# Performance work log

Measured on AMD Instinct MI355X. Metric: run time of the kernel, lower is better.

Reference implementation:

```python
import jax, jax.numpy as jnp
import numpy as np
import math

K, N, T, HID = 10, 96, 40, 48   # samples, agents (batch_size=1), timesteps, hidden
HZ = 10.0
R0, R1 = 0.5, 4.0
SPB = 6                          # social pooling grid is 6x6
RSTEP = (R1 - R0) / SPB          # radius_step (not set in shown source; natural value)
TWO_PI = 2.0 * math.pi
TSTEP = TWO_PI / SPB             # theta_step


def setup_inputs() -> dict:
    key = jax.random.key(0)
    ks = iter(jax.random.split(key, 24))
    def u(shape, fan):
        s = 1.0 / float(np.sqrt(fan))
        return jax.random.uniform(next(ks), shape, jnp.float32, -s, s)
    inp = {
        "hx": jax.random.normal(next(ks), (N, HID), jnp.float32),
        # locations in [-15,15] keep feature-map pixel gather in-bounds (u=40-long(y))
        "current_location": (jax.random.uniform(next(ks), (N, 2), jnp.float32) - 0.5) * 30.0,
        "y_path": (jax.random.uniform(next(ks), (K, T, N, 2), jnp.float32) - 0.5) * 30.0,
        "image_data": jax.random.normal(next(ks), (1, 4, 160, 160), jnp.float32),
        "conv1_w": u((16, 4, 5, 5), 4 * 25), "conv1_b": u((16,), 4 * 25),
        "conv2_w": u((32, 16, 5, 5), 16 * 25), "conv2_b": u((32,), 16 * 25),
        "fcvel_w": u((16, 2), 2), "fcvel_b": u((16,), 2),
        "gru_wih": u((3 * HID, 96), 96), "gru_whh": u((3 * HID, HID), HID),
        "gru_bih": u((3 * HID,), HID), "gru_bhh": u((3 * HID,), HID),
        "fcscf_w": u((HID, SPB * SPB * HID), SPB * SPB * HID), "fcscf_b": u((HID,), SPB * SPB * HID),
        "fcscore_w": u((1, HID), HID), "fcscore_b": u((1,), HID),
        "fcdy_w": u((2 * T, HID), HID), "fcdy_b": u((2 * T,), HID),
    }
    return inp


def _forward(hx, current_location, y_path, image_data, conv1_w, conv1_b, conv2_w, conv2_b,
             fcvel_w, fcvel_b, gru_wih, gru_whh, gru_bih, gru_bhh,
             fcscf_w, fcscf_b, fcscore_w, fcscore_b, fcdy_w, fcdy_b):
    # cnn_map: (1,4,160,160) -> (1,32,80,80)
    x = jax.lax.conv_general_dilated(image_data, conv1_w, (2, 2), ((2, 2), (2, 2)),
                                     dimension_numbers=("NCHW", "OIHW", "NCHW"))
    x = jax.nn.relu(x + conv1_b[None, :, None, None])
    x = jax.lax.conv_general_dilated(x, conv2_w, (1, 1), ((2, 2), (2, 2)),
                                     dimension_numbers=("NCHW", "OIHW", "NCHW"))
    fmap = jax.nn.relu(x + conv2_b[None, :, None, None])[0]  # (32,80,80); batch_size=1
    H = fmap.shape[1]

    # compute_vel + fc_vel: (K,T,N,2) -> (K,T,N,16)
    prev = jnp.concatenate([jnp.broadcast_to(current_location[None, None], (K, 1, N, 2)),
                            y_path[:, :-1]], axis=1)
    vel = (y_path - prev) * HZ
    y_fv = jax.nn.relu(vel @ fcvel_w.T + fcvel_b)

    hx_all = jnp.tile(hx, (K, 1))  # hx.repeat((K,1)) -> (K*N,48)
    t_idx = jnp.arange(N)
    not_self = ~jnp.eye(N, dtype=bool)

    def step(h, xs):
        loc, fv_t = xs  # (K,N,2), (K,N,16)
        hidden = h[:N]  # replicates hx[0:n] slice used in the original scf call
        # feature-map gather at agent pixel (.long() truncates toward zero)
        ui = (H // 2) - loc[..., 1].astype(jnp.int32)
        vi = (H // 2) - loc[..., 0].astype(jnp.int32)
        feat = jnp.moveaxis(fmap[:, ui, vi], 0, -1)  # (K,N,32)
        # pairwise dist/angle binning: c[k,j,t] = loc_t - loc_j
        c = loc[:, None, :, :] - loc[:, :, None, :]
        dist = jnp.linalg.norm(c, axis=-1)                        # (K,N,N)
        valid = (dist >= R0) & (dist <= R1) & not_self[None]
        dsafe = jnp.maximum(dist, 1e-10)
        cost = jnp.clip(c[..., 0] / dsafe, -1.0, 1.0)
        ac = jnp.arccos(cost)
        theta = jnp.where(c[..., 1] < 0, TWO_PI - ac, ac)
        ub = jnp.clip(((dist - R0) / RSTEP).astype(jnp.int32), 0, SPB - 1)
        vb = jnp.clip((theta / TSTEP).astype(jnp.int32), 0, SPB - 1)
        bins = ub * SPB + vb                                      # (K,N,N)
        hot = (bins[..., None] == jnp.arange(SPB * SPB)) & valid[..., None]  # (K,N,N,36)
        counts = hot.sum(axis=2)                                  # (K,N,36)
        # original writes hidden[t] with set() in increasing-t order: last writer = max t
        winner = jnp.max(jnp.where(hot, t_idx[None, None, :, None], -1), axis=2)
        sp = jnp.where(winner[..., None] >= 0, hidden[jnp.maximum(winner, 0)], 0.0)  # (K,N,36,48)
        sp = sp / jnp.maximum(counts, 1)[..., None]
        sps = sp.reshape(K, N, SPB * SPB * HID)
        lhalf = jnp.concatenate([feat, fv_t], axis=-1)            # (K,N,48)
        rhalf = jax.nn.relu(sps @ fcscf_w.T + fcscf_b)            # (K,N,48)
        x_i = jnp.concatenate([lhalf, rhalf], axis=-1).reshape(K * N, 96)
        # torch GRUCell (gate order r,z,n)
        gi = x_i @ gru_wih.T + gru_bih
        gh = h @ gru_whh.T + gru_bhh
        ir, iz, inn = jnp.split(gi, 3, axis=-1)
        hr, hz_, hn = jnp.split(gh, 3, axis=-1)
        r = jax.nn.sigmoid(ir + hr)
        z = jax.nn.sigmoid(iz + hz_)
        ng = jnp.tanh(inn + r * hn)
        h_new = (1.0 - z) * ng + z * h
        return h_new, h_new

    xs = (jnp.moveaxis(y_path, 1, 0), jnp.moveaxis(y_fv, 1, 0))  # time-major
    h_last, hs = jax.lax.scan(step, hx_all, xs)                  # hs: (T,K*N,48)
    delta_y = jax.nn.relu(h_last @ fcdy_w.T + fcdy_b)            # (K*N,80)
    delta_y = delta_y.reshape(K, N, 2, T).transpose(0, 3, 1, 2)  # (K,40,N,2)
    score = (hs @ fcscore_w.T + fcscore_b).sum(axis=0).reshape(K, N, 1)
    return delta_y, score


def reference(hx, current_location, y_path, image_data, conv1_w, conv1_b, conv2_w, conv2_b,
              fcvel_w, fcvel_b, gru_wih, gru_whh, gru_bih, gru_bhh,
              fcscf_w, fcscf_b, fcscore_w, fcscore_b, fcdy_w, fcdy_b):
    return _forward(hx, current_location, y_path, image_data, conv1_w, conv1_b, conv2_w, conv2_b,
                    fcvel_w, fcvel_b, gru_wih, gru_whh, gru_bih, gru_bhh,
                    fcscf_w, fcscf_b, fcscore_w, fcscore_b, fcdy_w, fcdy_b)
```

## Files before the change

kernel.cpp:

```cpp
#include <hip/hip_runtime.h>
#include <math.h>

#define KK 10
#define NN 96
#define TT 40

#define HZf 10.0f
#define R0f 0.5f
#define R1f 4.0f
#define RSTEPf ((4.0f - 0.5f) / 6.0f)
#define TWO_PIf 6.2831853071795864769f
#define TSTEPf (6.2831853071795864769f / 6.0f)

typedef unsigned short u16;
typedef unsigned int u32;
typedef unsigned long long u64;

__device__ __forceinline__ u16 f2bf(float f) {
    union { float f; unsigned u; } v; v.f = f;
    unsigned r = v.u + 0x7fffu + ((v.u >> 16) & 1u);
    return (u16)(r >> 16);
}
__device__ __forceinline__ float bflo(u32 u) {
    union { unsigned u; float f; } v; v.u = u << 16; return v.f;
}
__device__ __forceinline__ float bfhi(u32 u) {
    union { unsigned u; float f; } v; v.u = u & 0xffff0000u; return v.f;
}
__device__ __forceinline__ float bf2f(u16 h) {
    union { unsigned u; float f; } v; v.u = ((unsigned)h) << 16; return v.f;
}
__device__ __forceinline__ float sigmoidf_(float x) { return 1.0f / (1.0f + expf(-x)); }

__global__ void conv1_k(const float* __restrict__ img, const float* __restrict__ w,
                        const float* __restrict__ b, float* __restrict__ out) {
    int idx = blockIdx.x * blockDim.x + threadIdx.x;
    if (idx >= 16 * 80 * 80) return;
    int x = idx % 80, y = (idx / 80) % 80, o = idx / 6400;
    float acc = b[o];
    for (int c = 0; c < 4; c++)
        for (int ky = 0; ky < 5; ky++) {
            int iy = y * 2 + ky - 2;
            if (iy < 0 || iy >= 160) continue;
            for (int kx = 0; kx < 5; kx++) {
                int ix = x * 2 + kx - 2;
                if (ix < 0 || ix >= 160) continue;
                acc += img[(c * 160 + iy) * 160 + ix] * w[((o * 4 + c) * 5 + ky) * 5 + kx];
            }
        }
    out[idx] = fmaxf(acc, 0.0f);
}

__global__ void conv2_k(const float* __restrict__ in, const float* __restrict__ w,
                        const float* __restrict__ b, float* __restrict__ out) {
    int idx = blockIdx.x * blockDim.x + threadIdx.x;
    if (idx >= 32 * 80 * 80) return;
    int x = idx % 80, y = (idx / 80) % 80, o = idx / 6400;
    float acc = b[o];
    for (int c = 0; c < 16; c++)
        for (int ky = 0; ky < 5; ky++) {
            int iy = y + ky - 2;
            if (iy < 0 || iy >= 80) continue;
            for (int kx = 0; kx < 5; kx++) {
                int ix = x + kx - 2;
                if (ix < 0 || ix >= 80) continue;
                acc += in[(c * 80 + iy) * 80 + ix] * w[((o * 16 + c) * 5 + ky) * 5 + kx];
            }
        }
    out[idx] = fmaxf(acc, 0.0f);
}

__global__ void prep_w3(const float* __restrict__ scf, const float* __restrict__ wih,
                        const float* __restrict__ whh, const float* __restrict__ bih,
                        const float* __restrict__ bhh, const float* __restrict__ scfb,
                        const float* __restrict__ hx, float* __restrict__ h0hist,
                        u32* __restrict__ wscf_p, u32* __restrict__ Wr_p,
                        u32* __restrict__ Wz_p, u32* __restrict__ Win_p,
                        u32* __restrict__ Whn_p, float* __restrict__ bias5) {
    int idx = blockIdx.x * blockDim.x + threadIdx.x;
    if (idx < 41472) {
        int o = idx % 48, dp = (idx / 48) % 24, b = idx / 1152;
        float v0 = scf[o * 1728 + b * 48 + 2 * dp];
        float v1 = scf[o * 1728 + b * 48 + 2 * dp + 1];
        wscf_p[idx] = (u32)f2bf(v0) | ((u32)f2bf(v1) << 16);
    } else if (idx < 44928) {
        int j = idx - 41472, od = j % 48, dp = j / 48;
        int kk0 = 2 * dp, kk1 = 2 * dp + 1;
        float v0 = kk0 < 96 ? wih[od * 96 + kk0] : whh[od * 48 + kk0 - 96];
        float v1 = kk1 < 96 ? wih[od * 96 + kk1] : whh[od * 48 + kk1 - 96];
        Wr_p[j] = (u32)f2bf(v0) | ((u32)f2bf(v1) << 16);
    } else if (idx < 48384) {
        int j = idx - 44928, od = j % 48, dp = j / 48;
        int row = 48 + od, kk0 = 2 * dp, kk1 = 2 * dp + 1;
        float v0 = kk0 < 96 ? wih[row * 96 + kk0] : whh[row * 48 + kk0 - 96];
        float v1 = kk1 < 96 ? wih[row * 96 + kk1] : whh[row * 48 + kk1 - 96];
        Wz_p[j] = (u32)f2bf(v0) | ((u32)f2bf(v1) << 16);
    } else if (idx < 50688) {
        int j = idx - 48384, od = j % 48, dp = j / 48;
        int row = 96 + od;
        Win_p[j] = (u32)f2bf(wih[row * 96 + 2 * dp]) | ((u32)f2bf(wih[row * 96 + 2 * dp + 1]) << 16);
    } else if (idx < 51840) {
        int j = idx - 50688, od = j % 48, dp = j / 48;
        int row = 96 + od;
        Whn_p[j] = (u32)f2bf(whh[row * 48 + 2 * dp]) | ((u32)f2bf(whh[row * 48 + 2 * dp + 1]) << 16);
    } else if (idx < 52080) {
        int j = idx - 51840, od = j % 48, q = j / 48;
        float v;
        if (q == 0) v = bih[od] + bhh[od];
        else if (q == 1) v = bih[48 + od] + bhh[48 + od];
        else if (q == 2) v = bih[96 + od];
        else if (q == 3) v = bhh[96 + od];
        else v = scfb[od];
        bias5[j] = v;
    } else if (idx < 56688) {
        int j = idx - 52080;
        h0hist[j] = hx[j];
    }
}

__global__ void lhalf_k(const float* __restrict__ yp, const float* __restrict__ cur,
                        const float* __restrict__ fmap, const float* __restrict__ vw,
                        const float* __restrict__ vb, u16* __restrict__ lhalf_bf) {
    int item = blockIdx.x;
    int n = item % NN, k = (item / NN) % KK, t = item / (KK * NN);
    int lane = threadIdx.x;
    float lx = yp[((k * TT + t) * NN + n) * 2 + 0];
    float ly = yp[((k * TT + t) * NN + n) * 2 + 1];
    float px, py;
    if (t == 0) { px = cur[n * 2]; py = cur[n * 2 + 1]; }
    else { px = yp[((k * TT + t - 1) * NN + n) * 2]; py = yp[((k * TT + t - 1) * NN + n) * 2 + 1]; }
    float vx = (lx - px) * HZf, vy = (ly - py) * HZf;
    int ui = 40 - (int)ly;
    int vi = 40 - (int)lx;
    ui = min(max(ui, 0), 79);
    vi = min(max(vi, 0), 79);
    int row = k * NN + n;
    u16* dst = lhalf_bf + ((size_t)t * 960 + row) * 48;
    if (lane < 32) {
        dst[lane] = f2bf(fmap[(lane * 80 + ui) * 80 + vi]);
    } else if (lane < 48) {
        int f = lane - 32;
        float a = vb[f] + vx * vw[f * 2 + 0] + vy * vw[f * 2 + 1];
        dst[lane] = f2bf(fmaxf(a, 0.0f));
    }
}

__global__ __launch_bounds__(256) void bins4_k(const float* __restrict__ yp,
                                               u32* __restrict__ binc) {
    int tk = blockIdx.x;
    int k = tk % KK, t = tk / KK;
    int tid = threadIdx.x;
    __shared__ float xs[96], ys[96];
    __shared__ int win_s[96 * 36];
    __shared__ int cnt_s[96 * 36];
    if (tid < 96) {
        xs[tid] = yp[((k * TT + t) * NN + tid) * 2 + 0];
        ys[tid] = yp[((k * TT + t) * NN + tid) * 2 + 1];
    }
    for (int i = tid; i < 96 * 36; i += 256) { win_s[i] = -1; cnt_s[i] = 0; }
    __syncthreads();
    for (int p = tid; p < 96 * 96; p += 256) {
        int i = p / 96, j = p % 96;
        if (i == j) continue;
        float dx = xs[j] - xs[i], dy = ys[j] - ys[i];
        float dist = sqrtf(dx * dx + dy * dy);
        if (dist < R0f || dist > R1f) continue;
        float dsafe = fmaxf(dist, 1e-10f);
        float cost = fminf(fmaxf(dx / dsafe, -1.0f), 1.0f);
        float ac = acosf(cost);
        float theta = (dy < 0.0f) ? (TWO_PIf - ac) : ac;
        int ub = (int)((dist - R0f) / RSTEPf); ub = min(max(ub, 0), 5);
        int vb = (int)(theta / TSTEPf);        vb = min(max(vb, 0), 5);
        int b = ub * 6 + vb;
        atomicAdd(&cnt_s[i * 36 + b], 1);
        atomicMax(&win_s[i * 36 + b], j);
    }
    __syncthreads();
    if (tid < 96) {
        u32 base = (u32)(t * 960 + k * 96 + tid) * 20u;
        u16* entg = (u16*)(binc + base + 2);
        u64 mask = 0ull;
        int ne = 0;
        for (int b = 0; b < 36; ++b) {
            int w = win_s[tid * 36 + b];
            if (w >= 0) {
                mask |= 1ull << b;
                entg[ne++] = (u16)((w << 8) | cnt_s[tid * 36 + b]);
            }
        }
        binc[base] = (u32)mask;
        binc[base + 1] = (u32)(mask >> 32);
    }
}

__global__ __launch_bounds__(256) void step_k(
    int t, float* __restrict__ h0hist, const u16* __restrict__ lhalf_bf,
    const u32* __restrict__ binc, const u32* __restrict__ wscf_p,
    const u32* __restrict__ Wr_p, const u32* __restrict__ Wz_p,
    const u32* __restrict__ Win_p, const u32* __restrict__ Whn_p,
    const float* __restrict__ bias5, const float* __restrict__ scw,
    float* __restrict__ score_acc, float* __restrict__ hfin,
    u16* __restrict__ rhalf_all, const float* __restrict__ hx,
    float* __restrict__ hf) {
    __shared__ u32 smu[9856];
    float* smf = (float*)smu;
    const int tid = threadIdx.x;
    const int wv = tid >> 6, lane = tid & 63;
    const int lo = lane < 48 ? lane : 47;

    if (blockIdx.x < 96) {
        if (t >= TT) return;
        const float* hcur = h0hist + (size_t)t * 4608;
        const int r = blockIdx.x;
        float* shw = smf;
        float* shx = smf + 1728;
        float* ps1 = smf + 1872;
        float* ps2 = smf + 2064;
        u32* sent = (u32*)(smf + 2832);
        unsigned char* blist = (unsigned char*)(smf + 2852);

        if (tid < 20) sent[tid] = binc[(size_t)(t * 960 + r) * 20 + tid];
        if (tid < 48) {
            shx[tid] = bf2f(lhalf_bf[((size_t)t * 960 + r) * 48 + tid]);
            shx[96 + tid] = hcur[r * 48 + tid];
        }
        __syncthreads();
        u64 mask = ((u64)sent[1] << 32) | sent[0];
        int ne = __popcll(mask);
        const u16* ent = (const u16*)(sent + 2);
        if (tid < 36 && ((mask >> tid) & 1)) {
            int rank = __popcll(mask & ((1ull << tid) - 1ull));
            blist[rank] = (unsigned char)tid;
        }
        for (int i = tid; i < ne * 48; i += 256) {
            int e = i / 48, c = i - e * 48;
            int w = (ent[e] >> 8) & 0xff;
            shw[i] = hcur[w * 48 + c];
        }
        __syncthreads();
        float acc = 0.f;
        for (int e = 0; e < ne; ++e) {
            int b = blist[e];
            float cinv = 1.0f / (float)(ent[e] & 0xff);
            const u32* wp = wscf_p + (b * 24 + wv * 6) * 48 + lo;
            const float* xv = shw + e * 48 + wv * 12;
            float a = 0.f;
#pragma unroll
            for (int dp = 0; dp < 6; ++dp) {
                u32 u = wp[dp * 48];
                a += bflo(u) * xv[2 * dp] + bfhi(u) * xv[2 * dp + 1];
            }
            acc += a * cinv;
        }
        if (lane < 48) ps1[wv * 48 + lane] = acc;
        __syncthreads();
        if (wv == 0 && lane < 48) {
            float rh = ps1[lane] + ps1[48 + lane] + ps1[96 + lane] + ps1[144 + lane] +
                       bias5[192 + lane];
            shx[48 + lane] = fmaxf(rh, 0.f);
        }
        __syncthreads();
        float aR = 0.f, aZ = 0.f, aI = 0.f, aH = 0.f;
        int dp0 = wv * 18;
#pragma unroll
        for (int i = 0; i < 18; ++i) {
            int dp = dp0 + i;
            u32 uR = Wr_p[dp * 48 + lo], uZ = Wz_p[dp * 48 + lo];
            float xlo = shx[2 * dp], xhi = shx[2 * dp + 1];
            aR += bflo(uR) * xlo + bfhi(uR) * xhi;
            aZ += bflo(uZ) * xlo + bfhi(uZ) * xhi;
            if (dp < 48) {
                u32 uI = Win_p[dp * 48 + lo];
                aI += bflo(uI) * xlo + bfhi(uI) * xhi;
            } else {
                u32 uH = Whn_p[(dp - 48) * 48 + lo];
                aH += bflo(uH) * xlo + bfhi(uH) * xhi;
            }
        }
        if (lane < 48) {
            ps2[(wv * 4 + 0) * 48 + lane] = aR;
            ps2[(wv * 4 + 1) * 48 + lane] = aZ;
            ps2[(wv * 4 + 2) * 48 + lane] = aI;
            ps2[(wv * 4 + 3) * 48 + lane] = aH;
        }
        __syncthreads();
        if (wv == 0) {
            float sv = 0.f;
            if (lane < 48) {
                float AR = 0.f, AZ = 0.f, AI = 0.f, AH = 0.f;
#pragma unroll
                for (int w2 = 0; w2 < 4; ++w2) {
                    AR += ps2[(w2 * 4 + 0) * 48 + lane];
                    AZ += ps2[(w2 * 4 + 1) * 48 + lane];
                    AI += ps2[(w2 * 4 + 2) * 48 + lane];
                    AH += ps2[(w2 * 4 + 3) * 48 + lane];
                }
                float hprev = shx[96 + lane];
                float rr = sigmoidf_(AR + bias5[lane]);
                float zz = sigmoidf_(AZ + bias5[48 + lane]);
                float ng = tanhf(AI + bias5[96 + lane] + rr * (AH + bias5[144 + lane]));
                float hn = (1.0f - zz) * ng + zz * hprev;
                h0hist[(size_t)(t + 1) * 4608 + r * 48 + lane] = hn;
                if (t == TT - 1) hfin[r * 48 + lane] = hn;
                sv = hn * scw[lane];
            }
            for (int off = 32; off; off >>= 1) sv += __shfl_down(sv, off);
            if (lane == 0) score_acc[r] = (t == 0 ? 0.f : score_acc[r]) + sv;
        }
    } else if (blockIdx.x < 312) {
        if (t >= TT) return;
        const float* hcur = h0hist + (size_t)t * 4608;
        int widx = (blockIdx.x - 96) * 4 + wv;
        int row = 96 + widx;
        float* myw = smf + wv * 1728;
        const u32* bp = binc + (size_t)(t * 960 + row) * 20;
        u64 mask = ((u64)bp[1] << 32) | bp[0];
        int ne = __popcll(mask);
        const u16* ent = (const u16*)(bp + 2);
        for (int i = lane; i < ne * 48; i += 64) {
            int e = i / 48, c = i - e * 48;
            int w = (ent[e] >> 8) & 0xff;
            myw[i] = hcur[w * 48 + c];
        }
        __syncthreads();
        float acc = 0.f;
        u64 m2 = mask;
        for (int e = 0; e < ne; ++e) {
            int b = __ffsll((long long)m2) - 1;
            m2 &= m2 - 1;
            float cinv = 1.0f / (float)(ent[e] & 0xff);
            const u32* wp = wscf_p + b * 24 * 48 + lo;
            const float* xv = myw + e * 48;
            float a = 0.f;
#pragma unroll 8
            for (int dp = 0; dp < 24; ++dp) {
                u32 u = wp[dp * 48];
                a += bflo(u) * xv[2 * dp] + bfhi(u) * xv[2 * dp + 1];
            }
            acc += a * cinv;
        }
        float rh = fmaxf(acc + bias5[192 + lo], 0.f);
        if (lane < 48) rhalf_all[((size_t)t * 864 + widx) * 48 + lane] = f2bf(rh);
    } else {
        int s = t - 1;
        if (s < 0 || s >= TT) return;
        u32* sWr = smu;
        u32* sWz = smu + 3456;
        u32* sWin = smu + 6912;
        u32* sx = smu + 9216 + wv * 48;
        float* shh = (float*)(smu + 9408) + wv * 48;
        for (int i = tid; i < 3456; i += 256) { sWr[i] = Wr_p[i]; sWz[i] = Wz_p[i]; }
        for (int i = tid; i < 2304; i += 256) sWin[i] = Win_p[i];
        u32 whn[24];
#pragma unroll
        for (int dp = 0; dp < 24; ++dp) whn[dp] = Whn_p[dp * 48 + lo];
        int widx = (blockIdx.x - 312) * 4 + wv;
        int row = 96 + widx;
        const float* hsrc = (s == 0) ? (hx + (row % 96) * 48) : (hf + (s & 1) * 41472 + widx * 48);
        float hreg = hsrc[lo];
        if (lane < 24) {
            sx[lane] = *(const u32*)(lhalf_bf + ((size_t)s * 960 + row) * 48 + 2 * lane);
            sx[24 + lane] = *(const u32*)(rhalf_all + ((size_t)s * 864 + widx) * 48 + 2 * lane);
        }
        if (lane < 48) shh[lane] = hreg;
        __syncthreads();
        const float bRb = bias5[lo], bZb = bias5[48 + lo], bIb = bias5[96 + lo],
                    bHb = bias5[144 + lo];
        float aR = 0.f, aZ = 0.f, aI = 0.f, aH = 0.f;
#pragma unroll 8
        for (int dp = 0; dp < 48; ++dp) {
            u32 xp = sx[dp];
            float xlo = bflo(xp), xhi = bfhi(xp);
            u32 uR = sWr[dp * 48 + lo], uZ = sWz[dp * 48 + lo], uI = sWin[dp * 48 + lo];
            aR += bflo(uR) * xlo + bfhi(uR) * xhi;
            aZ += bflo(uZ) * xlo + bfhi(uZ) * xhi;
            aI += bflo(uI) * xlo + bfhi(uI) * xhi;
        }
#pragma unroll 8
        for (int dp = 48; dp < 72; ++dp) {
            float xlo = shh[2 * dp - 96], xhi = shh[2 * dp - 95];
            u32 uR = sWr[dp * 48 + lo], uZ = sWz[dp * 48 + lo], uH = whn[dp - 48];
            aR += bflo(uR) * xlo + bfhi(uR) * xhi;
            aZ += bflo(uZ) * xlo + bfhi(uZ) * xhi;
            aH += bflo(uH) * xlo + bfhi(uH) * xhi;
        }
        float rr = sigmoidf_(aR + bRb);
        float zz = sigmoidf_(aZ + bZb);
        float ng = tanhf(aI + bIb + rr * (aH + bHb));
        float hn = (1.0f - zz) * ng + zz * hreg;
        if (lane < 48) {
            hf[((s + 1) & 1) * 41472 + widx * 48 + lane] = hn;
            if (s == TT - 1) hfin[(size_t)row * 48 + lane] = hn;
        }
        float sv = (lane < 48) ? hn * scw[lane] : 0.f;
        for (int off = 32; off; off >>= 1) sv += __shfl_down(sv, off);
        if (lane == 0) score_acc[row] = (s == 0 ? 0.f : score_acc[row]) + sv;
    }
}

__global__ void final_k(const float* __restrict__ hlast, const float* __restrict__ score_acc,
                        const float* __restrict__ dyw, const float* __restrict__ dyb,
                        const float* __restrict__ scoreb, float* __restrict__ out) {
    int row = blockIdx.x, lane = threadIdx.x;
    int n = row % 96, k = row / 96;
    __shared__ float sh_h[48];
    if (lane < 48) sh_h[lane] = hlast[row * 48 + lane];
    __syncthreads();
    if (lane < 80) {
        float a = dyb[lane];
#pragma unroll 8
        for (int d = 0; d < 48; d++) a += sh_h[d] * dyw[lane * 48 + d];
        a = fmaxf(a, 0.0f);
        int j = lane / 40, tt = lane % 40;
        out[((k * TT + tt) * NN + n) * 2 + j] = a;
    } else if (lane == 80) {
        out[76800 + row] = score_acc[row] + 40.0f * scoreb[0];
    }
}

extern "C" void kernel_launch(void* const* d_in, const int* in_sizes, int n_in,
                              void* d_out, int out_size, void* d_ws, size_t ws_size,
                              hipStream_t stream) {
    const float* hx  = (const float*)d_in[0];
    const float* cur = (const float*)d_in[1];
    const float* yp  = (const float*)d_in[2];
    const float* img = (const float*)d_in[3];
    const float* c1w = (const float*)d_in[4];
    const float* c1b = (const float*)d_in[5];
    const float* c2w = (const float*)d_in[6];
    const float* c2b = (const float*)d_in[7];
    const float* vw  = (const float*)d_in[8];
    const float* vb  = (const float*)d_in[9];
    const float* wih = (const float*)d_in[10];
    const float* whh = (const float*)d_in[11];
    const float* bih = (const float*)d_in[12];
    const float* bhh = (const float*)d_in[13];
    const float* scfw = (const float*)d_in[14];
    const float* scfb = (const float*)d_in[15];
    const float* scw  = (const float*)d_in[16];
    const float* scb  = (const float*)d_in[17];
    const float* dyw  = (const float*)d_in[18];
    const float* dyb  = (const float*)d_in[19];
    float* out = (float*)d_out;

    char* ws = (char*)d_ws;
    u32*   binc     = (u32*)(ws + 0);
    float* fmap1    = (float*)(ws + 0);
    float* fmap     = (float*)(ws + 409600);
    u16*   rhalf_all= (u16*)(ws + 3072000);
    u16*   lhalf_bf = (u16*)(ws + 6389760);
    float* h0hist   = (float*)(ws + 10076160);
    float* hfin     = (float*)(ws + 10831872);
    float* score_acc= (float*)(ws + 11016192);
    u32*   wscf_p   = (u32*)(ws + 11020032);
    u32*   Wr_p     = (u32*)(ws + 11185920);
    u32*   Wz_p     = (u32*)(ws + 11199744);
    u32*   Win_p    = (u32*)(ws + 11213568);
    u32*   Whn_p    = (u32*)(ws + 11222784);
    float* bias5    = (float*)(ws + 11227392);
    float* hf       = (float*)(ws + 11228352);

    conv1_k<<<400, 256, 0, stream>>>(img, c1w, c1b, fmap1);
    conv2_k<<<800, 256, 0, stream>>>(fmap1, c2w, c2b, fmap);
    prep_w3<<<222, 256, 0, stream>>>(scfw, wih, whh, bih, bhh, scfb, hx, h0hist,
                                     wscf_p, Wr_p, Wz_p, Win_p, Whn_p, bias5);
    lhalf_k<<<TT * KK * NN, 64, 0, stream>>>(yp, cur, fmap, vw, vb, lhalf_bf);
    bins4_k<<<TT * KK, 256, 0, stream>>>(yp, binc);

    for (int t = 0; t <= TT; ++t) {
        step_k<<<528, 256, 0, stream>>>(t, h0hist, lhalf_bf, binc, wscf_p, Wr_p, Wz_p,
                                        Win_p, Whn_p, bias5, scw, score_acc, hfin,
                                        rhalf_all, hx, hf);
    }
    final_k<<<960, 128, 0, stream>>>(hfin, score_acc, dyw, dyb, scb, out);
}
```

Baseline: 534.2 us.

## Tile convolutions through shared memory and pack four lhalf items per block

Replaces the naive per-output conv1/conv2 kernels with 8x8 spatial tiles that stage the input halo and all weights in LDS. Each thread computes 4 or 8 output channels using vectorized weight reads, which cuts redundant global loads. The lhalf kernel now processes four items per 256-thread block instead of one per 64-thread block, reducing block count. The tiled convs launch only 100 blocks, so fewer CUs are busy, and conv2 loads a 50KB weight table into LDS in every block.

```diff
diff --git a/kernel.cpp b/kernel.cpp
--- a/kernel.cpp
+++ b/kernel.cpp
@@ -15,6 +15,7 @@
 typedef unsigned short u16;
 typedef unsigned int u32;
 typedef unsigned long long u64;
+typedef float f32x4 __attribute__((ext_vector_type(4)));
 
 __device__ __forceinline__ u16 f2bf(float f) {
     union { float f; unsigned u; } v; v.f = f;
@@ -32,42 +33,96 @@
 }
 __device__ __forceinline__ float sigmoidf_(float x) { return 1.0f / (1.0f + expf(-x)); }
 
-__global__ void conv1_k(const float* __restrict__ img, const float* __restrict__ w,
-                        const float* __restrict__ b, float* __restrict__ out) {
-    int idx = blockIdx.x * blockDim.x + threadIdx.x;
-    if (idx >= 16 * 80 * 80) return;
-    int x = idx % 80, y = (idx / 80) % 80, o = idx / 6400;
-    float acc = b[o];
-    for (int c = 0; c < 4; c++)
-        for (int ky = 0; ky < 5; ky++) {
-            int iy = y * 2 + ky - 2;
-            if (iy < 0 || iy >= 160) continue;
-            for (int kx = 0; kx < 5; kx++) {
-                int ix = x * 2 + kx - 2;
-                if (ix < 0 || ix >= 160) continue;
-                acc += img[(c * 160 + iy) * 160 + ix] * w[((o * 4 + c) * 5 + ky) * 5 + kx];
-            }
-        }
-    out[idx] = fmaxf(acc, 0.0f);
-}
-
-__global__ void conv2_k(const float* __restrict__ in, const float* __restrict__ w,
-                        const float* __restrict__ b, float* __restrict__ out) {
-    int idx = blockIdx.x * blockDim.x + threadIdx.x;
-    if (idx >= 32 * 80 * 80) return;
-    int x = idx % 80, y = (idx / 80) % 80, o = idx / 6400;
-    float acc = b[o];
-    for (int c = 0; c < 16; c++)
-        for (int ky = 0; ky < 5; ky++) {
-            int iy = y + ky - 2;
-            if (iy < 0 || iy >= 80) continue;
-            for (int kx = 0; kx < 5; kx++) {
-                int ix = x + kx - 2;
-                if (ix < 0 || ix >= 80) continue;
-                acc += in[(c * 80 + iy) * 80 + ix] * w[((o * 16 + c) * 5 + ky) * 5 + kx];
-            }
-        }
-    out[idx] = fmaxf(acc, 0.0f);
+__global__ __launch_bounds__(256) void conv1_t(const float* __restrict__ img,
+                                               const float* __restrict__ w,
+                                               const float* __restrict__ b,
+                                               float* __restrict__ out) {
+    __shared__ float sW[1600];
+    __shared__ float sIn[1444];
+    const int tid = threadIdx.x;
+    const int bx = blockIdx.x % 10, by = blockIdx.x / 10;
+    const int x0 = bx * 8, y0 = by * 8;
+    for (int i = tid; i < 1600; i += 256) {
+        int oc = i & 15, t2 = i >> 4, tap = t2 % 25, ic = t2 / 25;
+        sW[i] = w[(oc * 4 + ic) * 25 + tap];
+    }
+    for (int i = tid; i < 1444; i += 256) {
+        int ic = i / 361, rem = i % 361, r = rem / 19, c = rem % 19;
+        int gy = 2 * y0 - 2 + r, gx = 2 * x0 - 2 + c;
+        sIn[i] = (gy >= 0 && gy < 160 && gx >= 0 && gx < 160)
+                     ? img[(ic * 160 + gy) * 160 + gx] : 0.f;
+    }
+    __syncthreads();
+    const int pix = tid & 63, ocg = tid >> 6;
+    const int px = pix & 7, py = pix >> 3;
+    float acc[4];
+#pragma unroll
+    for (int j = 0; j < 4; ++j) acc[j] = b[ocg * 4 + j];
+#pragma unroll
+    for (int ic = 0; ic < 4; ++ic) {
+        int ibase = ic * 361;
+#pragma unroll
+        for (int ky = 0; ky < 5; ++ky) {
+#pragma unroll
+            for (int kx = 0; kx < 5; ++kx) {
+                float iv = sIn[ibase + (2 * py + ky) * 19 + 2 * px + kx];
+                f32x4 wv = *(const f32x4*)&sW[(ic * 25 + ky * 5 + kx) * 16 + ocg * 4];
+#pragma unroll
+                for (int j = 0; j < 4; ++j) acc[j] += iv * wv[j];
+            }
+        }
+    }
+#pragma unroll
+    for (int j = 0; j < 4; ++j)
+        out[((ocg * 4 + j) * 80 + y0 + py) * 80 + x0 + px] = fmaxf(acc[j], 0.f);
+}
+
+__global__ __launch_bounds__(256) void conv2_t(const float* __restrict__ in,
+                                               const float* __restrict__ w,
+                                               const float* __restrict__ b,
+                                               float* __restrict__ out) {
+    __shared__ float sW[12800];
+    __shared__ float sIn[2304];
+    const int tid = threadIdx.x;
+    const int bx = blockIdx.x % 10, by = blockIdx.x / 10;
+    const int x0 = bx * 8, y0 = by * 8;
+    for (int i = tid; i < 12800; i += 256) {
+        int oc = i & 31, t2 = i >> 5, tap = t2 % 25, ic = t2 / 25;
+        sW[i] = w[(oc * 16 + ic) * 25 + tap];
+    }
+    for (int i = tid; i < 2304; i += 256) {
+        int ic = i / 144, rem = i % 144, r = rem / 12, c = rem % 12;
+        int gy = y0 - 2 + r, gx = x0 - 2 + c;
+        sIn[i] = (gy >= 0 && gy < 80 && gx >= 0 && gx < 80)
+                     ? in[(ic * 80 + gy) * 80 + gx] : 0.f;
+    }
+    __syncthreads();
+    const int pix = tid & 63, ocg = tid >> 6;
+    const int px = pix & 7, py = pix >> 3;
+    float acc[8];
+#pragma unroll
+    for (int j = 0; j < 8; ++j) acc[j] = b[ocg * 8 + j];
+    for (int ic = 0; ic < 16; ++ic) {
+        int ibase = ic * 144;
+#pragma unroll
+        for (int ky = 0; ky < 5; ++ky) {
+#pragma unroll
+            for (int kx = 0; kx < 5; ++kx) {
+                float iv = sIn[ibase + (py + ky) * 12 + px + kx];
+                int wb = (ic * 25 + ky * 5 + kx) * 32 + ocg * 8;
+                f32x4 w0 = *(const f32x4*)&sW[wb];
+                f32x4 w1 = *(const f32x4*)&sW[wb + 4];
+#pragma unroll
+                for (int j = 0; j < 4; ++j) {
+                    acc[j] += iv * w0[j];
+                    acc[4 + j] += iv * w1[j];
+                }
+            }
+        }
+    }
+#pragma unroll
+    for (int j = 0; j < 8; ++j)
+        out[((ocg * 8 + j) * 80 + y0 + py) * 80 + x0 + px] = fmaxf(acc[j], 0.f);
 }
 
 __global__ void prep_w3(const float* __restrict__ scf, const float* __restrict__ wih,
@@ -118,12 +173,15 @@
     }
 }
 
-__global__ void lhalf_k(const float* __restrict__ yp, const float* __restrict__ cur,
-                        const float* __restrict__ fmap, const float* __restrict__ vw,
-                        const float* __restrict__ vb, u16* __restrict__ lhalf_bf) {
-    int item = blockIdx.x;
+__global__ __launch_bounds__(256) void lhalf_k(const float* __restrict__ yp,
+                                               const float* __restrict__ cur,
+                                               const float* __restrict__ fmap,
+                                               const float* __restrict__ vw,
+                                               const float* __restrict__ vb,
+                                               u16* __restrict__ lhalf_bf) {
+    int item = blockIdx.x * 4 + (threadIdx.x >> 6);
+    int lane = threadIdx.x & 63;
     int n = item % NN, k = (item / NN) % KK, t = item / (KK * NN);
-    int lane = threadIdx.x;
     float lx = yp[((k * TT + t) * NN + n) * 2 + 0];
     float ly = yp[((k * TT + t) * NN + n) * 2 + 1];
     float px, py;
@@ -460,11 +518,11 @@
     float* bias5    = (float*)(ws + 11227392);
     float* hf       = (float*)(ws + 11228352);
 
-    conv1_k<<<400, 256, 0, stream>>>(img, c1w, c1b, fmap1);
-    conv2_k<<<800, 256, 0, stream>>>(fmap1, c2w, c2b, fmap);
+    conv1_t<<<100, 256, 0, stream>>>(img, c1w, c1b, fmap1);
+    conv2_t<<<100, 256, 0, stream>>>(fmap1, c2w, c2b, fmap);
     prep_w3<<<222, 256, 0, stream>>>(scfw, wih, whh, bih, bhh, scfb, hx, h0hist,
                                      wscf_p, Wr_p, Wz_p, Win_p, Whn_p, bias5);
-    lhalf_k<<<TT * KK * NN, 64, 0, stream>>>(yp, cur, fmap, vw, vb, lhalf_bf);
+    lhalf_k<<<TT * KK * NN / 4, 256, 0, stream>>>(yp, cur, fmap, vw, vb, lhalf_bf);
     bins4_k<<<TT * KK, 256, 0, stream>>>(yp, binc);
 
     for (int t = 0; t <= TT; ++t) {
```

After: 490.1 us. -8.3%, faster.
